# Kernel optimization log

Measured on AMD Instinct MI355X. Metric: run time of the kernel, lower is better.

## Reference

```python
import jax, jax.numpy as jnp
import numpy as np

N_NODES = 50000
N_EDGES = 800000
NFEAT = 128
NHID = 128


def gcn_conv(x, edge_index, W, b):
    """PyG GCNConv: add self-loops, symmetric deg^-1/2 normalization, scatter-add."""
    n = x.shape[0]
    loop = jnp.arange(n, dtype=edge_index.dtype)
    row = jnp.concatenate([edge_index[0], loop])  # source nodes
    col = jnp.concatenate([edge_index[1], loop])  # target nodes
    ones = jnp.ones(row.shape[0], dtype=x.dtype)
    deg = jax.ops.segment_sum(ones, col, num_segments=n)
    dinv = jnp.where(deg > 0, jax.lax.rsqrt(deg), 0.0).astype(x.dtype)
    norm = dinv[row] * dinv[col]  # [E+N]
    h = x @ W  # [n, out]
    msg = h[row] * norm[:, None]  # gather + scale, [E+N, out]
    out = jax.ops.segment_sum(msg, col, num_segments=n)  # scatter-add
    return out + b


def setup_inputs() -> dict:
    key = jax.random.key(0)
    kx, ke, k1, k2 = jax.random.split(key, 4)
    x = jax.random.normal(kx, (N_NODES, NFEAT), dtype=jnp.float32)
    edge_index = jax.random.randint(ke, (2, N_EDGES), 0, N_NODES, dtype=jnp.int32)
    s1 = 1.0 / np.sqrt(NFEAT)
    s2 = 1.0 / np.sqrt(NHID)
    W1 = jax.random.uniform(k1, (NFEAT, NHID), jnp.float32, -s1, s1)
    b1 = jnp.zeros((NHID,), jnp.float32)
    W2 = jax.random.uniform(k2, (NHID, NHID), jnp.float32, -s2, s2)
    b2 = jnp.zeros((NHID,), jnp.float32)
    return {"x": x, "edge_index": edge_index, "W1": W1, "b1": b1, "W2": W2, "b2": b2}


def reference(x, edge_index, W1, b1, W2, b2):
    # DGI.forward -> encoder z: relu(GCNConv) x2, dropout=0, no layernorm
    h = jax.nn.relu(gcn_conv(x, edge_index, W1, b1))
    z = jax.nn.relu(gcn_conv(h, edge_index, W2, b2))
    return z
```

## Files before the change

kernel.cpp:

```cpp
#include <hip/hip_runtime.h>
#include <hip/hip_fp16.h>


#define NBK 98
#define BSH 9
#define BCAP 10240

typedef _Float16 f16x8 __attribute__((ext_vector_type(8)));
typedef float f32x4 __attribute__((ext_vector_type(4)));

__global__ __launch_bounds__(256) void k_bucket(const int* __restrict__ row,
                                                const int* __restrict__ col,
                                                int* __restrict__ bcur,
                                                unsigned int* __restrict__ arena,
                                                int E) {
  __shared__ int hist[NBK];
  __shared__ int basec[NBK];
  int tid = threadIdx.x;
  if (tid < NBK) hist[tid] = 0;
  __syncthreads();
  int base = blockIdx.x * 2048;
  int cc[8], rr[8], bb[8];
#pragma unroll
  for (int j = 0; j < 8; ++j) {
    int e = base + j * 256 + tid;
    bb[j] = -1;
    if (e < E) {
      cc[j] = col[e];
      rr[j] = row[e];
      bb[j] = cc[j] >> BSH;
      atomicAdd(&hist[bb[j]], 1);
    }
  }
  __syncthreads();
  if (tid < NBK && hist[tid] > 0)
    basec[tid] = atomicAdd(&bcur[tid], hist[tid]);
  __syncthreads();
#pragma unroll
  for (int j = 0; j < 8; ++j) {
    if (bb[j] >= 0) {
      int pos = atomicAdd(&basec[bb[j]], 1);
      if (pos < BCAP)
        arena[(size_t)bb[j] * BCAP + pos] =
            ((unsigned int)rr[j] << BSH) | (unsigned int)(cc[j] & 511);
    }
  }
}

__global__ __launch_bounds__(256) void k_bhist(const int* __restrict__ bcur,
                                               const unsigned int* __restrict__ arena,
                                               int* __restrict__ cnt,
                                               float* __restrict__ dinv, int n) {
  __shared__ int h[512];
  int b = blockIdx.x, tid = threadIdx.x;
  h[tid] = 0;
  h[tid + 256] = 0;
  __syncthreads();
  int m = min(bcur[b], BCAP);
  int nb0 = b << BSH;
  const unsigned int* a = arena + (size_t)b * BCAP;
  for (int i = tid; i < m; i += 256) atomicAdd(&h[a[i] & 511], 1);
  __syncthreads();
  for (int t = tid; t < 512; t += 256) {
    int node = nb0 + t;
    if (node < n) {
      cnt[node] = h[t];
      dinv[node] = rsqrtf((float)(h[t] + 1));
    }
  }
}

__global__ __launch_bounds__(512) void k_scan1(const int* __restrict__ cnt,
                                               int* __restrict__ offs,
                                               int* __restrict__ bsum, int n) {
  __shared__ int s[512];
  int t = threadIdx.x;
  int i = blockIdx.x * 512 + t;
  int v = (i < n) ? cnt[i] : 0;
  s[t] = v;
  __syncthreads();
#pragma unroll
  for (int d = 1; d < 512; d <<= 1) {
    int add = (t >= d) ? s[t - d] : 0;
    __syncthreads();
    s[t] += add;
    __syncthreads();
  }
  if (i < n) offs[i] = s[t] - v;
  if (t == 511) bsum[blockIdx.x] = s[511];
}

__global__ __launch_bounds__(128) void k_scan2(const int* __restrict__ bsum,
                                               int* __restrict__ bsumsc, int nb) {
  __shared__ int s[128];
  int t = threadIdx.x;
  int v = (t < nb) ? bsum[t] : 0;
  s[t] = v;
  __syncthreads();
#pragma unroll
  for (int d = 1; d < 128; d <<= 1) {
    int add = (t >= d) ? s[t - d] : 0;
    __syncthreads();
    s[t] += add;
    __syncthreads();
  }
  if (t < nb) bsumsc[t] = s[t] - v;
}

__global__ __launch_bounds__(256) void k_scan3(int* __restrict__ offs,
                                               const int* __restrict__ bsumsc,
                                               int n, int E) {
  int i = blockIdx.x * 256 + threadIdx.x;
  if (i < n) offs[i] += bsumsc[i >> 9];
  else if (i == n) offs[n] = E;
}

__global__ __launch_bounds__(256) void k_bscatter(const int* __restrict__ bcur,
                                                  const unsigned int* __restrict__ arena,
                                                  const int* __restrict__ offs,
                                                  int* __restrict__ esrc, int n) {
  __shared__ int cur[512];
  int b = blockIdx.x, tid = threadIdx.x;
  int nb0 = b << BSH;
  for (int t = tid; t < 512; t += 256) {
    int node = nb0 + t;
    cur[t] = (node < n) ? offs[node] : 0;
  }
  __syncthreads();
  int m = min(bcur[b], BCAP);
  const unsigned int* a = arena + (size_t)b * BCAP;
  for (int i = tid; i < m; i += 256) {
    unsigned int p = a[i];
    int pos = atomicAdd(&cur[p & 511], 1);
    esrc[pos] = (int)(p >> BSH);
  }
}

__global__ __launch_bounds__(256) void k_prepW(const float* __restrict__ W1,
                                               const float* __restrict__ W2,
                                               __half* __restrict__ Wt1,
                                               __half* __restrict__ Wt2) {
  int i = blockIdx.x * 256 + threadIdx.x;
  int n = i >> 7, k = i & 127;
  Wt1[i] = (__half)W1[k * 128 + n];
  Wt2[i] = (__half)W2[k * 128 + n];
}

__device__ inline uint4 loadA16(const float* A, int grow, int k16, int M) {
  if (grow >= M) return make_uint4(0, 0, 0, 0);
  const float4* p = (const float4*)(A + (size_t)grow * 128 + k16 * 8);
  float4 f0 = p[0], f1 = p[1];
  __half2 h0 = __floats2half2_rn(f0.x, f0.y);
  __half2 h1 = __floats2half2_rn(f0.z, f0.w);
  __half2 h2 = __floats2half2_rn(f1.x, f1.y);
  __half2 h3 = __floats2half2_rn(f1.z, f1.w);
  uint4 u;
  u.x = *(unsigned int*)&h0;
  u.y = *(unsigned int*)&h1;
  u.z = *(unsigned int*)&h2;
  u.w = *(unsigned int*)&h3;
  return u;
}
__device__ inline uint4 loadA16(const __half* A, int grow, int k16, int M) {
  if (grow >= M) return make_uint4(0, 0, 0, 0);
  return *(const uint4*)(A + (size_t)grow * 128 + k16 * 8);
}

template <typename AT>
__global__ __launch_bounds__(256) void k_gemm(const AT* __restrict__ A,
                                              const __half* __restrict__ Wt,
                                              const float* __restrict__ dinv,
                                              __half* __restrict__ C, int M) {
  __shared__ char smem[16384 + 32768];
  char* Al = smem;
  char* Bl = smem + 16384;
  int tid = threadIdx.x;
  int row0 = blockIdx.x * 64;

  const uint4* Wt4 = (const uint4*)Wt;
#pragma unroll
  for (int i = 0; i < 8; ++i) {
    int c = tid + 256 * i;
    int n = c >> 4, k16 = c & 15;
    uint4 v = Wt4[c];
    *(uint4*)(Bl + n * 256 + ((k16 * 16) ^ ((n & 7) << 4))) = v;
  }
#pragma unroll
  for (int i = 0; i < 4; ++i) {
    int c = tid + 256 * i;
    int r = c >> 4, k16 = c & 15;
    uint4 v = loadA16(A, row0 + r, k16, M);
    *(uint4*)(Al + r * 256 + ((k16 * 16) ^ ((r & 7) << 4))) = v;
  }
  __syncthreads();

  int w = tid >> 6, l = tid & 63;
  int lr = l & 15, lq = l >> 4;
  f32x4 acc[8] = {};
#pragma unroll
  for (int kc = 0; kc < 4; ++kc) {
    int c16 = kc * 4 + lq;
    int ar = w * 16 + lr;
    f16x8 av = *(const f16x8*)(Al + ar * 256 + ((c16 * 16) ^ ((lr & 7) << 4)));
#pragma unroll
    for (int nt = 0; nt < 8; ++nt) {
      int n = nt * 16 + lr;
      f16x8 bv = *(const f16x8*)(Bl + n * 256 + ((c16 * 16) ^ ((n & 7) << 4)));
      acc[nt] = __builtin_amdgcn_mfma_f32_16x16x32_f16(av, bv, acc[nt], 0, 0, 0);
    }
  }

  int orow = row0 + w * 16 + lq * 4;
#pragma unroll
  for (int r = 0; r < 4; ++r) {
    int grow = orow + r;
    if (grow < M) {
      float dv = dinv[grow];
#pragma unroll
      for (int nt = 0; nt < 8; ++nt)
        C[(size_t)grow * 128 + nt * 16 + lr] = (__half)(acc[nt][r] * dv);
    }
  }
}

template <bool FP16OUT>
__global__ __launch_bounds__(256) void k_agg(const __half* __restrict__ hs,
                                             const int* __restrict__ offs,
                                             const int* __restrict__ esrc,
                                             const float* __restrict__ dinv,
                                             const float* __restrict__ bias,
                                             void* __restrict__ outp, int n) {
  int gw = (blockIdx.x * 256 + threadIdx.x) >> 6;
  int lane = threadIdx.x & 63;
  if (gw >= n) return;
  float di = dinv[gw];
  const unsigned int* base = (const unsigned int*)hs;
  unsigned int su = base[(size_t)gw * 64 + lane];
  float2 v = __half22float2(*(__half2*)&su);
  float ax = v.x, ay = v.y;
  int e0 = offs[gw], e1 = offs[gw + 1];
  int e = e0;
  for (; e + 16 <= e1; e += 16) {
    int s[16];
#pragma unroll
    for (int j = 0; j < 16; ++j) s[j] = esrc[e + j];
    unsigned int u[16];
#pragma unroll
    for (int j = 0; j < 16; ++j) u[j] = base[(size_t)s[j] * 64 + lane];
#pragma unroll
    for (int j = 0; j < 16; ++j) {
      float2 hv = __half22float2(*(__half2*)&u[j]);
      ax += hv.x;
      ay += hv.y;
    }
  }
  for (; e + 4 <= e1; e += 4) {
    int s[4];
#pragma unroll
    for (int j = 0; j < 4; ++j) s[j] = esrc[e + j];
    unsigned int u[4];
#pragma unroll
    for (int j = 0; j < 4; ++j) u[j] = base[(size_t)s[j] * 64 + lane];
#pragma unroll
    for (int j = 0; j < 4; ++j) {
      float2 hv = __half22float2(*(__half2*)&u[j]);
      ax += hv.x;
      ay += hv.y;
    }
  }
  for (; e < e1; ++e) {
    unsigned int u = base[(size_t)esrc[e] * 64 + lane];
    float2 hv = __half22float2(*(__half2*)&u);
    ax += hv.x;
    ay += hv.y;
  }
  float2 bv = ((const float2*)bias)[lane];
  float ox = fmaxf(fmaf(ax, di, bv.x), 0.f);
  float oy = fmaxf(fmaf(ay, di, bv.y), 0.f);
  if (FP16OUT) {
    __half2 p = __floats2half2_rn(ox, oy);
    ((unsigned int*)outp)[(size_t)gw * 64 + lane] = *(unsigned int*)&p;
  } else {
    ((float2*)outp)[(size_t)gw * 64 + lane] = make_float2(ox, oy);
  }
}

extern "C" void kernel_launch(void* const* d_in, const int* in_sizes, int n_in,
                              void* d_out, int out_size, void* d_ws, size_t ws_size,
                              hipStream_t stream) {
  const float* x  = (const float*)d_in[0];
  const int*   ei = (const int*)d_in[1];
  const float* W1 = (const float*)d_in[2];
  const float* b1 = (const float*)d_in[3];
  const float* W2 = (const float*)d_in[4];
  const float* b2 = (const float*)d_in[5];
  const int n = in_sizes[0] / 128;
  const int E = in_sizes[1] / 2;
  const int* row = ei;
  const int* col = ei + E;

  char* ws = (char*)d_ws;
  size_t off = 0;
  auto alloc = [&](size_t bytes) -> void* {
    void* p = ws + off;
    off = (off + bytes + 255) & ~(size_t)255;
    return p;
  };
  int*          cnt    = (int*)alloc((size_t)n * 4);
  int*          offs   = (int*)alloc((size_t)(n + 1) * 4);
  float*        dinv   = (float*)alloc((size_t)n * 4);
  int*          bsum   = (int*)alloc(4096);
  int*          bsumsc = (int*)alloc(4096);
  int*          bcur   = (int*)alloc(NBK * 4);
  int*          esrc   = (int*)alloc((size_t)E * 4);
  unsigned int* arena  = (unsigned int*)alloc((size_t)NBK * BCAP * 4);
  __half*       Wt1    = (__half*)alloc(128 * 128 * 2);
  __half*       Wt2    = (__half*)alloc(128 * 128 * 2);
  __half*       h_tmp  = (__half*)alloc((size_t)n * 128 * 2);
  __half*       h16    = (__half*)alloc((size_t)n * 128 * 2);
  (void)ws_size; (void)n_in; (void)out_size;

  hipMemsetAsync(bcur, 0, NBK * 4, stream);
  k_bucket<<<(E + 2047) / 2048, 256, 0, stream>>>(row, col, bcur, arena, E);
  k_bhist<<<NBK, 256, 0, stream>>>(bcur, arena, cnt, dinv, n);
  const int nb = (n + 511) / 512;
  k_scan1<<<nb, 512, 0, stream>>>(cnt, offs, bsum, n);
  k_scan2<<<1, 128, 0, stream>>>(bsum, bsumsc, nb);
  k_scan3<<<(n + 1 + 255) / 256, 256, 0, stream>>>(offs, bsumsc, n, E);
  k_bscatter<<<NBK, 256, 0, stream>>>(bcur, arena, offs, esrc, n);

  k_prepW<<<64, 256, 0, stream>>>(W1, W2, Wt1, Wt2);

  const int gb = (n + 63) / 64;
  const int ab = (n * 64 + 255) / 256;
  k_gemm<float><<<gb, 256, 0, stream>>>(x, Wt1, dinv, h_tmp, n);
  k_agg<true><<<ab, 256, 0, stream>>>(h_tmp, offs, esrc, dinv, b1, h16, n);
  k_gemm<__half><<<gb, 256, 0, stream>>>(h16, Wt2, dinv, h_tmp, n);
  k_agg<false><<<ab, 256, 0, stream>>>(h_tmp, offs, esrc, dinv, b2, d_out, n);
}
```

Baseline: 153.2 us.

## Fuse histogram, scan and scatter into a single per-bucket CSR kernel

Replaces the bucket histogram, three-pass global scan and bucket scatter kernels with one k_csr kernel. Each bucket block computes its global base by reducing the sizes of the preceding buckets, then runs a local scan to get node offsets and scatters edges. The bcur memset is folded into k_prepW, which now runs first. This removes five launches and the intermediate cnt/bsum round trips, at the cost of each block redundantly reducing up to NBK bucket counts.

```diff
diff --git a/kernel.cpp b/kernel.cpp
--- a/kernel.cpp
+++ b/kernel.cpp
@@ -47,91 +47,65 @@
   }
 }
 
-__global__ __launch_bounds__(256) void k_bhist(const int* __restrict__ bcur,
-                                               const unsigned int* __restrict__ arena,
-                                               int* __restrict__ cnt,
-                                               float* __restrict__ dinv, int n) {
-  __shared__ int h[512];
+__global__ __launch_bounds__(256) void k_csr(const int* __restrict__ bcur,
+                                             const unsigned int* __restrict__ arena,
+                                             int* __restrict__ offs,
+                                             float* __restrict__ dinv,
+                                             int* __restrict__ esrc, int n) {
+  __shared__ int hist[512];
+  __shared__ int psum[256];
   int b = blockIdx.x, tid = threadIdx.x;
-  h[tid] = 0;
-  h[tid + 256] = 0;
-  __syncthreads();
-  int m = min(bcur[b], BCAP);
-  int nb0 = b << BSH;
-  const unsigned int* a = arena + (size_t)b * BCAP;
-  for (int i = tid; i < m; i += 256) atomicAdd(&h[a[i] & 511], 1);
-  __syncthreads();
-  for (int t = tid; t < 512; t += 256) {
-    int node = nb0 + t;
-    if (node < n) {
-      cnt[node] = h[t];
-      dinv[node] = rsqrtf((float)(h[t] + 1));
-    }
-  }
-}
-
-__global__ __launch_bounds__(512) void k_scan1(const int* __restrict__ cnt,
-                                               int* __restrict__ offs,
-                                               int* __restrict__ bsum, int n) {
-  __shared__ int s[512];
-  int t = threadIdx.x;
-  int i = blockIdx.x * 512 + t;
-  int v = (i < n) ? cnt[i] : 0;
-  s[t] = v;
-  __syncthreads();
-#pragma unroll
-  for (int d = 1; d < 512; d <<= 1) {
-    int add = (t >= d) ? s[t - d] : 0;
-    __syncthreads();
-    s[t] += add;
-    __syncthreads();
-  }
-  if (i < n) offs[i] = s[t] - v;
-  if (t == 511) bsum[blockIdx.x] = s[511];
-}
-
-__global__ __launch_bounds__(128) void k_scan2(const int* __restrict__ bsum,
-                                               int* __restrict__ bsumsc, int nb) {
-  __shared__ int s[128];
-  int t = threadIdx.x;
-  int v = (t < nb) ? bsum[t] : 0;
-  s[t] = v;
-  __syncthreads();
-#pragma unroll
-  for (int d = 1; d < 128; d <<= 1) {
-    int add = (t >= d) ? s[t - d] : 0;
-    __syncthreads();
-    s[t] += add;
-    __syncthreads();
-  }
-  if (t < nb) bsumsc[t] = s[t] - v;
-}
-
-__global__ __launch_bounds__(256) void k_scan3(int* __restrict__ offs,
-                                               const int* __restrict__ bsumsc,
-                                               int n, int E) {
-  int i = blockIdx.x * 256 + threadIdx.x;
-  if (i < n) offs[i] += bsumsc[i >> 9];
-  else if (i == n) offs[n] = E;
-}
-
-__global__ __launch_bounds__(256) void k_bscatter(const int* __restrict__ bcur,
-                                                  const unsigned int* __restrict__ arena,
-                                                  const int* __restrict__ offs,
-                                                  int* __restrict__ esrc, int n) {
-  __shared__ int cur[512];
-  int b = blockIdx.x, tid = threadIdx.x;
-  int nb0 = b << BSH;
-  for (int t = tid; t < 512; t += 256) {
-    int node = nb0 + t;
-    cur[t] = (node < n) ? offs[node] : 0;
-  }
+  hist[tid] = 0;
+  hist[tid + 256] = 0;
   __syncthreads();
   int m = min(bcur[b], BCAP);
   const unsigned int* a = arena + (size_t)b * BCAP;
+  for (int i = tid; i < m; i += 256) atomicAdd(&hist[a[i] & 511], 1);
+  __syncthreads();
+
+  psum[tid] = (tid < b && tid < NBK) ? min(bcur[tid], BCAP) : 0;
+  __syncthreads();
+#pragma unroll
+  for (int d = 128; d > 0; d >>= 1) {
+    if (tid < d) psum[tid] += psum[tid + d];
+    __syncthreads();
+  }
+  int base = psum[0];
+  __syncthreads();
+
+  int a0 = hist[2 * tid], a1 = hist[2 * tid + 1];
+  int pair = a0 + a1;
+  psum[tid] = pair;
+  __syncthreads();
+#pragma unroll
+  for (int d = 1; d < 256; d <<= 1) {
+    int add = (tid >= d) ? psum[tid - d] : 0;
+    __syncthreads();
+    psum[tid] += add;
+    __syncthreads();
+  }
+  int excl = psum[tid] - pair;
+  int o0 = base + excl, o1 = o0 + a0;
+
+  int nb0 = b << BSH;
+  int node0 = nb0 + 2 * tid, node1 = node0 + 1;
+  if (node0 < n) {
+    offs[node0] = o0;
+    dinv[node0] = rsqrtf((float)(a0 + 1));
+  }
+  if (node1 < n) {
+    offs[node1] = o1;
+    dinv[node1] = rsqrtf((float)(a1 + 1));
+  }
+  if (b == NBK - 1 && tid == 255) offs[n] = base + psum[255];
+  __syncthreads();
+
+  hist[2 * tid] = o0;
+  hist[2 * tid + 1] = o1;
+  __syncthreads();
   for (int i = tid; i < m; i += 256) {
     unsigned int p = a[i];
-    int pos = atomicAdd(&cur[p & 511], 1);
+    int pos = atomicAdd(&hist[p & 511], 1);
     esrc[pos] = (int)(p >> BSH);
   }
 }
@@ -139,11 +113,13 @@
 __global__ __launch_bounds__(256) void k_prepW(const float* __restrict__ W1,
                                                const float* __restrict__ W2,
                                                __half* __restrict__ Wt1,
-                                               __half* __restrict__ Wt2) {
+                                               __half* __restrict__ Wt2,
+                                               int* __restrict__ bcur) {
   int i = blockIdx.x * 256 + threadIdx.x;
   int n = i >> 7, k = i & 127;
   Wt1[i] = (__half)W1[k * 128 + n];
   Wt2[i] = (__half)W2[k * 128 + n];
+  if (i < NBK) bcur[i] = 0;
 }
 
 __device__ inline uint4 loadA16(const float* A, int grow, int k16, int M) {
@@ -306,30 +282,20 @@
     off = (off + bytes + 255) & ~(size_t)255;
     return p;
   };
-  int*          cnt    = (int*)alloc((size_t)n * 4);
-  int*          offs   = (int*)alloc((size_t)(n + 1) * 4);
-  float*        dinv   = (float*)alloc((size_t)n * 4);
-  int*          bsum   = (int*)alloc(4096);
-  int*          bsumsc = (int*)alloc(4096);
-  int*          bcur   = (int*)alloc(NBK * 4);
-  int*          esrc   = (int*)alloc((size_t)E * 4);
-  unsigned int* arena  = (unsigned int*)alloc((size_t)NBK * BCAP * 4);
-  __half*       Wt1    = (__half*)alloc(128 * 128 * 2);
-  __half*       Wt2    = (__half*)alloc(128 * 128 * 2);
-  __half*       h_tmp  = (__half*)alloc((size_t)n * 128 * 2);
-  __half*       h16    = (__half*)alloc((size_t)n * 128 * 2);
+  int*          offs  = (int*)alloc((size_t)(n + 1) * 4);
+  float*        dinv  = (float*)alloc((size_t)n * 4);
+  int*          bcur  = (int*)alloc(NBK * 4);
+  int*          esrc  = (int*)alloc((size_t)E * 4);
+  unsigned int* arena = (unsigned int*)alloc((size_t)NBK * BCAP * 4);
+  __half*       Wt1   = (__half*)alloc(128 * 128 * 2);
+  __half*       Wt2   = (__half*)alloc(128 * 128 * 2);
+  __half*       h_tmp = (__half*)alloc((size_t)n * 128 * 2);
+  __half*       h16   = (__half*)alloc((size_t)n * 128 * 2);
   (void)ws_size; (void)n_in; (void)out_size;
 
-  hipMemsetAsync(bcur, 0, NBK * 4, stream);
+  k_prepW<<<64, 256, 0, stream>>>(W1, W2, Wt1, Wt2, bcur);
   k_bucket<<<(E + 2047) / 2048, 256, 0, stream>>>(row, col, bcur, arena, E);
-  k_bhist<<<NBK, 256, 0, stream>>>(bcur, arena, cnt, dinv, n);
-  const int nb = (n + 511) / 512;
-  k_scan1<<<nb, 512, 0, stream>>>(cnt, offs, bsum, n);
-  k_scan2<<<1, 128, 0, stream>>>(bsum, bsumsc, nb);
-  k_scan3<<<(n + 1 + 255) / 256, 256, 0, stream>>>(offs, bsumsc, n, E);
-  k_bscatter<<<NBK, 256, 0, stream>>>(bcur, arena, offs, esrc, n);
-
-  k_prepW<<<64, 256, 0, stream>>>(W1, W2, Wt1, Wt2);
+  k_csr<<<NBK, 256, 0, stream>>>(bcur, arena, offs, dinv, esrc, n);
 
   const int gb = (n + 63) / 64;
   const int ab = (n * 64 + 255) / 256;
```

New measurement: 139.7 us. -8.8%, faster.
